# Kernel tuning notes

Hardware: AMD Instinct MI355X
Metric: run time of the kernel (lower is better)

## Reference

```python
import jax, jax.numpy as jnp
import numpy as np

S, B, D, L = 100, 2048, 128, 2  # seq_len, batch, dim_model, n_layers
LN_EPS = 1e-5


def _layer_norm(x, g, b):
    # x: [S, B, D]; normalize over last dim (nn.LayerNorm(dim))
    mu = jnp.mean(x, axis=-1, keepdims=True)
    var = jnp.mean(jnp.square(x - mu), axis=-1, keepdims=True)
    return (x - mu) * jax.lax.rsqrt(var + LN_EPS) * g + b


def _asb(x, cw, cwh, thr):
    # Adaptive_Spectral_Block. x: [S, B, D] -> permute to [B, N, C]
    xb = jnp.transpose(x, (1, 0, 2)).astype(jnp.float32)  # [B, N, C]
    N = xb.shape[1]
    x_fft = jnp.fft.rfft(xb, axis=1, norm='ortho')  # [B, F, C] complex, F = N//2+1
    w = jax.lax.complex(cw[:, 0], cw[:, 1])          # [C]
    x_weighted = x_fft * w
    # adaptive high-frequency mask
    energy = jnp.sum(jnp.square(jnp.abs(x_fft)), axis=-1)  # [B, F]
    F = energy.shape[1]
    # torch.median returns the LOWER of the two middle values -> k-th smallest, k=(F-1)//2
    median = jnp.sort(energy, axis=1)[:, (F - 1) // 2][:, None]  # [B, 1]
    norm_e = energy / (median + 1e-6)
    threshold = jnp.quantile(norm_e, thr)  # global scalar quantile (linear interp, as torch)
    mask = (norm_e < threshold)[..., None].astype(x_fft.real.dtype)  # [B, F, 1]
    wh = jax.lax.complex(cwh[:, 0], cwh[:, 1])       # [C]
    x_weighted = x_weighted + (x_fft * mask) * wh
    out = jnp.fft.irfft(x_weighted, n=N, axis=1, norm='ortho')  # [B, N, C]
    return jnp.transpose(out, (1, 0, 2)).astype(x.dtype)  # back to [S, B, D]


def setup_inputs() -> dict:
    key = jax.random.key(0)
    k0, k1, k2, k3 = jax.random.split(key, 4)
    return {
        'x': jax.random.normal(k0, (S, B, D), dtype=jnp.float32),
        'complex_weight': jax.random.normal(k1, (L, D, 2), dtype=jnp.float32) * 0.02,
        'complex_weight_high': jax.random.normal(k2, (L, D, 2), dtype=jnp.float32) * 0.02,
        'threshold_param': jax.random.uniform(k3, (L,), dtype=jnp.float32) * 0.5,
        'gamma': jnp.ones((L, D), dtype=jnp.float32),
        'beta': jnp.zeros((L, D), dtype=jnp.float32),
    }


def reference(x, complex_weight, complex_weight_high, threshold_param, gamma, beta):
    # Encoder.forward: nlayers x (x = x + ASB(LayerNorm(x)))
    for i in range(L):
        h = _layer_norm(x, gamma[i], beta[i])
        x = x + _asb(h, complex_weight[i], complex_weight_high[i], threshold_param[i])
    return x
```

## Files before the change

kernel.cpp:

```cpp
#include <hip/hip_runtime.h>
#include <math.h>

#define SEQ    100
#define BATCH  2048
#define DIM    128
#define NF     51
#define NLAYER 2
#define MTOT   (BATCH * NF)
#define BD     (BATCH * DIM)
#define XSTR   16384
#define NBQ    96

typedef __attribute__((ext_vector_type(8))) short bf16x8;
typedef __attribute__((ext_vector_type(4))) float f32x4v;

__device__ __forceinline__ unsigned cvtpk(float lo, float hi) {
    unsigned r;
    asm("v_cvt_pk_bf16_f32 %0, %1, %2" : "=v"(r) : "v"(lo), "v"(hi));
    return r;
}
__device__ __forceinline__ unsigned short f2bf(float f) {
    unsigned u = __float_as_uint(f);
    return (unsigned short)((u + 0x7FFFu + ((u >> 16) & 1u)) >> 16);
}
__device__ __forceinline__ float bf2f(unsigned short u) {
    return __uint_as_float((unsigned)u << 16);
}

__global__ void k_tables(unsigned short* __restrict__ imgF,
                         unsigned short* __restrict__ imgI) {
    const int i = blockIdx.x * 256 + threadIdx.x;
    const float W = 6.28318530717958647692f / 100.f;
    if (i < 2 * 64 * 128) {
        const int p = i >> 13, k = (i >> 7) & 63, n = i & 127;
        float v = 0.f;
        if (k < NF && n < SEQ) {
            float s, c; sincosf((float)((k * n) % 100) * W, &s, &c);
            v = 0.1f * (p ? -s : c);
        }
        imgF[i] = f2bf(v);
    }
    if (i < 2 * 128 * 64) {
        const int p = i >> 13, n = (i >> 6) & 127, k = i & 63;
        float v = 0.f;
        if (k < NF && n < SEQ) {
            float s, c; sincosf((float)((k * n) % 100) * W, &s, &c);
            const float a = (k == 0 || k == 50) ? 0.1f : 0.2f;
            v = p ? -a * s : a * c;
        }
        imgI[i] = f2bf(v);
    }
}

__device__ __forceinline__ void fwd_mfma_tail(
    unsigned short* hT, const unsigned short* __restrict__ imgF,
    unsigned short* __restrict__ Xg, float* __restrict__ normE,
    int b, int t, int lane, int wv, int g4, int cc)
{
    bf16x8 Bf[2][4];
    #pragma unroll
    for (int ct = 0; ct < 2; ++ct) {
        const int c = wv * 32 + ct * 16 + cc;
        #pragma unroll
        for (int ks = 0; ks < 4; ++ks)
            Bf[ct][ks] = *(const bf16x8*)&hT[c * 128 + (((ks * 4 + g4) ^ (cc >> 1)) << 3)];
    }
    __syncthreads();

    float* epart    = (float*)hT;
    float* energy_s = (float*)hT + 256;
    float* medp     = (float*)hT + 320;

    #pragma unroll
    for (int mt = 0; mt < 4; ++mt) {
        const int kr = mt * 16 + cc;
        f32x4v aR[2], aI[2];
        aR[0] = aR[1] = aI[0] = aI[1] = (f32x4v){0.f, 0.f, 0.f, 0.f};
        #pragma unroll
        for (int ks = 0; ks < 4; ++ks) {
            const int e0 = kr * 128 + ks * 32 + g4 * 8;
            const bf16x8 A0 = *(const bf16x8*)&imgF[e0];
            const bf16x8 A1 = *(const bf16x8*)&imgF[8192 + e0];
            #pragma unroll
            for (int ct = 0; ct < 2; ++ct) {
                aR[ct] = __builtin_amdgcn_mfma_f32_16x16x32_bf16(A0, Bf[ct][ks], aR[ct], 0, 0, 0);
                aI[ct] = __builtin_amdgcn_mfma_f32_16x16x32_bf16(A1, Bf[ct][ks], aI[ct], 0, 0, 0);
            }
        }
        #pragma unroll
        for (int reg = 0; reg < 4; ++reg) {
            float e = aR[0][reg] * aR[0][reg] + aI[0][reg] * aI[0][reg]
                    + aR[1][reg] * aR[1][reg] + aI[1][reg] * aI[1][reg];
            e += __shfl_xor(e, 1, 64); e += __shfl_xor(e, 2, 64);
            e += __shfl_xor(e, 4, 64); e += __shfl_xor(e, 8, 64);
            if (cc == 0) epart[(mt * 16 + g4 * 4 + reg) * 4 + wv] = e;
        }
        #pragma unroll
        for (int ct = 0; ct < 2; ++ct) {
            const int c = wv * 32 + ct * 16 + cc;
            unsigned short* Xb = Xg + (size_t)b * XSTR + (size_t)c * 128;
            const int k0 = mt * 16 + g4 * 4;
            uint2 pr, pi;
            pr.x = cvtpk(aR[ct][0], aR[ct][1]); pr.y = cvtpk(aR[ct][2], aR[ct][3]);
            pi.x = cvtpk(aI[ct][0], aI[ct][1]); pi.y = cvtpk(aI[ct][2], aI[ct][3]);
            *(uint2*)&Xb[k0]      = pr;
            *(uint2*)&Xb[64 + k0] = pi;
        }
    }
    __syncthreads();
    if (t < 64) energy_s[t] = epart[4 * t] + epart[4 * t + 1]
                            + epart[4 * t + 2] + epart[4 * t + 3];
    __syncthreads();
    if (t < NF) {
        const float e = energy_s[t];
        int cnt = 0;
        for (int j = 0; j < NF; ++j) {
            const float ej = energy_s[j];
            cnt += (ej < e || (ej == e && j < t)) ? 1 : 0;
        }
        if (cnt == (NF - 1) / 2) *medp = e;
    }
    __syncthreads();
    if (t < NF) normE[b * NF + t] = energy_s[t] / (*medp + 1e-6f);
}

__global__ __launch_bounds__(256, 5) void k_fwd(
    const float* __restrict__ x,
    const float* __restrict__ gamma, const float* __restrict__ beta,
    const unsigned short* __restrict__ imgF,
    unsigned short* __restrict__ Xg,
    float* __restrict__ normE)
{
    __shared__ __align__(16) unsigned short hT[128 * 128];

    const int b = blockIdx.x, t = threadIdx.x;
    const int lane = t & 63, wv = t >> 6, g4 = lane >> 4, cc = lane & 15;

    {
        const int c0 = lane * 2;
        const float2 gv = *(const float2*)&gamma[c0];
        const float2 bv = *(const float2*)&beta[c0];
        float2 v[4][8];
        #pragma unroll
        for (int slot = 0; slot < 4; ++slot) {
            const int n0 = (slot * 4 + wv) * 8;
            #pragma unroll
            for (int j = 0; j < 8; ++j)
                if (n0 + j < SEQ)
                    v[slot][j] = *(const float2*)&x[(size_t)(n0 + j) * BD + (size_t)b * DIM + c0];
        }
        #pragma unroll
        for (int slot = 0; slot < 4; ++slot) {
            const int chunk = slot * 4 + wv;
            const int n0 = chunk * 8;
            float he[8], ho[8];
            #pragma unroll
            for (int j = 0; j < 8; ++j) {
                he[j] = 0.f; ho[j] = 0.f;
                if (n0 + j < SEQ) {
                    float s  = v[slot][j].x + v[slot][j].y;
                    float s2 = fmaf(v[slot][j].x, v[slot][j].x, v[slot][j].y * v[slot][j].y);
                    #pragma unroll
                    for (int off = 1; off < 64; off <<= 1) {
                        s  += __shfl_xor(s,  off, 64);
                        s2 += __shfl_xor(s2, off, 64);
                    }
                    const float mu   = s * (1.f / 128.f);
                    const float rstd = rsqrtf(s2 * (1.f / 128.f) - mu * mu + 1e-5f);
                    he[j] = fmaf((v[slot][j].x - mu) * rstd, gv.x, bv.x);
                    ho[j] = fmaf((v[slot][j].y - mu) * rstd, gv.y, bv.y);
                }
            }
            int4 ve, vo;
            ve.x = (int)cvtpk(he[0], he[1]); ve.y = (int)cvtpk(he[2], he[3]);
            ve.z = (int)cvtpk(he[4], he[5]); ve.w = (int)cvtpk(he[6], he[7]);
            vo.x = (int)cvtpk(ho[0], ho[1]); vo.y = (int)cvtpk(ho[2], ho[3]);
            vo.z = (int)cvtpk(ho[4], ho[5]); vo.w = (int)cvtpk(ho[6], ho[7]);
            const int sw = (chunk ^ (lane & 7)) << 3;
            *(int4*)&hT[(c0    ) * 128 + sw] = ve;
            *(int4*)&hT[(c0 + 1) * 128 + sw] = vo;
        }
    }
    __syncthreads();
    fwd_mfma_tail(hT, imgF, Xg, normE, b, t, lane, wv, g4, cc);
}

__device__ __forceinline__ void gbar(unsigned* slot) {
    __syncthreads();
    __threadfence();
    if (threadIdx.x == 0) {
        __hip_atomic_fetch_add(slot, 1u, __ATOMIC_ACQ_REL, __HIP_MEMORY_SCOPE_AGENT);
        while (__hip_atomic_load(slot, __ATOMIC_ACQUIRE, __HIP_MEMORY_SCOPE_AGENT) < NBQ)
            __builtin_amdgcn_s_sleep(8);
    }
    __syncthreads();
}

__device__ __forceinline__ void scan2(const unsigned* __restrict__ H0,
                                      int bins, int shift, bool entry,
                                      unsigned r0, unsigned* sp, unsigned* sc)
{
    const int t = threadIdx.x;
    if (t < 128) {
        const int j = t >> 6, ln = t & 63;
        const unsigned rk = r0 + (unsigned)j;
        const unsigned oldsp = entry ? sp[j] : 0u;
        const unsigned oldsc = entry ? sc[j] : 0u;
        const unsigned rem = rk - oldsc;
        const unsigned* H = H0 + (entry ? j * bins : 0);
        const int per = bins / 64;
        unsigned sum = 0;
        for (int i = 0; i < per; ++i)
            sum += __hip_atomic_load(&H[ln * per + i], __ATOMIC_RELAXED, __HIP_MEMORY_SCOPE_AGENT);
        unsigned pre = sum;
        #pragma unroll
        for (int off = 1; off < 64; off <<= 1) {
            const unsigned tt = __shfl_up(pre, off, 64);
            if (ln >= off) pre += tt;
        }
        const unsigned excl = pre - sum;
        if (rem >= excl && rem < excl + sum) {
            unsigned cum = excl;
            for (int i = 0; i < per; ++i) {
                const unsigned hc = __hip_atomic_load(&H[ln * per + i],
                                        __ATOMIC_RELAXED, __HIP_MEMORY_SCOPE_AGENT);
                if (rem < cum + hc) {
                    sp[j] = oldsp | ((unsigned)(ln * per + i) << shift);
                    sc[j] = oldsc + cum;
                    break;
                }
                cum += hc;
            }
        }
    }
    __syncthreads();
}

__global__ void k_quant(const float* __restrict__ normE,
                        unsigned* __restrict__ hist,
                        unsigned* __restrict__ counters,
                        const float* __restrict__ thrp,
                        const int layer,
                        float* __restrict__ thresh)
{
    __shared__ unsigned lh[4096];
    __shared__ unsigned sp[2], sc[2];
    const int t = threadIdx.x, bid = blockIdx.x;
    const float q = thrp[layer] * (float)(MTOT - 1);
    const unsigned r0 = (unsigned)floorf(q);
    unsigned* cnt = counters + layer * 4;

    for (int i = bid * 256 + t; i < 8192; i += NBQ * 256) hist[i] = 0u;
    gbar(cnt + 0);

    for (int i = t; i < 2048; i += 256) lh[i] = 0;
    __syncthreads();
    for (int i = bid * 256 + t; i < MTOT; i += NBQ * 256)
        atomicAdd(&lh[__float_as_uint(normE[i]) >> 21], 1u);
    __syncthreads();
    for (int i = t; i < 2048; i += 256) {
        const unsigned c = lh[i];
        if (c) atomicAdd(&hist[i], c);
    }
    gbar(cnt + 1);

    scan2(hist, 2048, 21, false, r0, sp, sc);
    {
        const unsigned p0 = sp[0], p1 = sp[1];
        for (int i = t; i < 4096; i += 256) lh[i] = 0;
        __syncthreads();
        for (int i = bid * 256 + t; i < MTOT; i += NBQ * 256) {
            const unsigned v = __float_as_uint(normE[i]);
            const unsigned bin = (v >> 10) & 2047u;
            if ((v & 0xFFE00000u) == p0) atomicAdd(&lh[bin], 1u);
            if ((v & 0xFFE00000u) == p1) atomicAdd(&lh[2048 + bin], 1u);
        }
        __syncthreads();
        for (int i = t; i < 4096; i += 256) {
            const unsigned c = lh[i];
            if (c) atomicAdd(&hist[2048 + i], c);
        }
    }
    gbar(cnt + 2);

    scan2(hist + 2048, 2048, 10, true, r0, sp, sc);
    {
        const unsigned p0 = sp[0], p1 = sp[1];
        for (int i = t; i < 2048; i += 256) lh[i] = 0;
        __syncthreads();
        for (int i = bid * 256 + t; i < MTOT; i += NBQ * 256) {
            const unsigned v = __float_as_uint(normE[i]);
            const unsigned bin = v & 1023u;
            if ((v & 0xFFFFFC00u) == p0) atomicAdd(&lh[bin], 1u);
            if ((v & 0xFFFFFC00u) == p1) atomicAdd(&lh[1024 + bin], 1u);
        }
        __syncthreads();
        for (int i = t; i < 2048; i += 256) {
            const unsigned c = lh[i];
            if (c) atomicAdd(&hist[6144 + i], c);
        }
    }
    gbar(cnt + 3);

    if (bid == 0) {
        scan2(hist + 6144, 1024, 0, true, r0, sp, sc);
        if (t == 0) {
            const float v0 = __uint_as_float(sp[0]);
            const float v1 = __uint_as_float(sp[1]);
            const float frac = q - floorf(q);
            thresh[0] = v0 * (1.f - frac) + v1 * frac;
        }
    }
}

__global__ __launch_bounds__(256, 4) void k_asb_fwd(
    const float* __restrict__ x,
    const float* __restrict__ cw, const float* __restrict__ cwh,
    const unsigned short* __restrict__ imgI,
    const unsigned short* __restrict__ imgF,
    const float* __restrict__ gamma_n, const float* __restrict__ beta_n,
    float* __restrict__ normE,
    const float* __restrict__ thresh,
    float* __restrict__ out,
    unsigned short* __restrict__ Xg)
{
    __shared__ __align__(16) unsigned short hT[128 * 128];
    __shared__ float mask_s[64];
    __shared__ float part_s[112][4], part_q[112][4];
    __shared__ float2 musv[112];

    const int b = blockIdx.x, t = threadIdx.x;
    const int lane = t & 63, wv = t >> 6, g4 = lane >> 4, cc = lane & 15;

    if (t < 64) mask_s[t] = (t < NF && normE[b * NF + t] < thresh[0]) ? 1.f : 0.f;
    __syncthreads();

    bf16x8 Yr[2][2], Yi[2][2];
    float gn[2], bn[2];
    #pragma unroll
    for (int ct = 0; ct < 2; ++ct) {
        const int c = wv * 32 + ct * 16 + cc;
        gn[ct] = gamma_n[c]; bn[ct] = beta_n[c];
        const unsigned short* Xb = Xg + (size_t)b * XSTR + (size_t)c * 128;
        const float2 w2 = *(const float2*)&cw[2 * c];
        const float2 h2 = *(const float2*)&cwh[2 * c];
        #pragma unroll
        for (int kb = 0; kb < 2; ++kb) {
            const bf16x8 xr = *(const bf16x8*)&Xb[kb * 32 + g4 * 8];
            const bf16x8 xi = *(const bf16x8*)&Xb[64 + kb * 32 + g4 * 8];
            float yr[8], yi[8];
            #pragma unroll
            for (int j = 0; j < 8; ++j) {
                const float m   = mask_s[kb * 32 + g4 * 8 + j];
                const float fre = fmaf(m, h2.x, w2.x);
                const float fim = fmaf(m, h2.y, w2.y);
                const float fxr = bf2f((unsigned short)xr[j]);
                const float fxi = bf2f((unsigned short)xi[j]);
                yr[j] = fxr * fre - fxi * fim;
                yi[j] = fxr * fim + fxi * fre;
            }
            unsigned ur[4], ui[4];
            #pragma unroll
            for (int jj = 0; jj < 4; ++jj) {
                ur[jj] = cvtpk(yr[2 * jj], yr[2 * jj + 1]);
                ui[jj] = cvtpk(yi[2 * jj], yi[2 * jj + 1]);
            }
            Yr[ct][kb] = *(bf16x8*)ur;
            Yi[ct][kb] = *(bf16x8*)ui;
        }
    }

    float ov[7][2][4];
    #pragma unroll
    for (int mt = 0; mt < 7; ++mt) {
        const int nr = mt * 16 + cc;
        f32x4v o[2];
        o[0] = o[1] = (f32x4v){0.f, 0.f, 0.f, 0.f};
        #pragma unroll
        for (int kb = 0; kb < 2; ++kb) {
            const int e0 = nr * 64 + kb * 32 + g4 * 8;
            const bf16x8 A0 = *(const bf16x8*)&imgI[e0];
            const bf16x8 A1 = *(const bf16x8*)&imgI[8192 + e0];
            #pragma unroll
            for (int ct = 0; ct < 2; ++ct) {
                o[ct] = __builtin_amdgcn_mfma_f32_16x16x32_bf16(A0, Yr[ct][kb], o[ct], 0, 0, 0);
                o[ct] = __builtin_amdgcn_mfma_f32_16x16x32_bf16(A1, Yi[ct][kb], o[ct], 0, 0, 0);
            }
        }
        #pragma unroll
        for (int ct = 0; ct < 2; ++ct) {
            const int c = wv * 32 + ct * 16 + cc;
            #pragma unroll
            for (int reg = 0; reg < 4; ++reg) {
                const int n = mt * 16 + g4 * 4 + reg;
                float val = 0.f;
                if (n < SEQ) {
                    const size_t idx = (size_t)n * BD + (size_t)b * DIM + c;
                    val = x[idx] + o[ct][reg];
                    out[idx] = val;
                }
                ov[mt][ct][reg] = val;
            }
        }
    }

    #pragma unroll
    for (int mt = 0; mt < 7; ++mt) {
        #pragma unroll
        for (int reg = 0; reg < 4; ++reg) {
            float s  = ov[mt][0][reg] + ov[mt][1][reg];
            float s2 = fmaf(ov[mt][0][reg], ov[mt][0][reg],
                            ov[mt][1][reg] * ov[mt][1][reg]);
            s  += __shfl_xor(s, 1, 64);  s  += __shfl_xor(s, 2, 64);
            s  += __shfl_xor(s, 4, 64);  s  += __shfl_xor(s, 8, 64);
            s2 += __shfl_xor(s2, 1, 64); s2 += __shfl_xor(s2, 2, 64);
            s2 += __shfl_xor(s2, 4, 64); s2 += __shfl_xor(s2, 8, 64);
            if (cc == 0) {
                const int n = mt * 16 + g4 * 4 + reg;
                part_s[n][wv] = s; part_q[n][wv] = s2;
            }
        }
    }
    __syncthreads();
    if (t < 112) {
        const float s  = part_s[t][0] + part_s[t][1] + part_s[t][2] + part_s[t][3];
        const float sq = part_q[t][0] + part_q[t][1] + part_q[t][2] + part_q[t][3];
        const float mu = s * (1.f / 128.f);
        const float rstd = rsqrtf(sq * (1.f / 128.f) - mu * mu + 1e-5f);
        musv[t] = make_float2(mu, rstd);
    }
    __syncthreads();

    {
        const int cf = t >> 1, chf = 14 + (t & 1);
        *(int4*)&hT[cf * 128 + ((chf ^ ((cf >> 1) & 7)) << 3)] = (int4){0, 0, 0, 0};
    }
    #pragma unroll
    for (int mt = 0; mt < 7; ++mt) {
        #pragma unroll
        for (int ct = 0; ct < 2; ++ct) {
            const int c = wv * 32 + ct * 16 + cc;
            #pragma unroll
            for (int pr = 0; pr < 2; ++pr) {
                const int n0 = mt * 16 + g4 * 4 + pr * 2;
                float h0 = 0.f, h1 = 0.f;
                if (n0 < SEQ) {
                    const float2 ms = musv[n0];
                    h0 = fmaf((ov[mt][ct][pr * 2] - ms.x) * ms.y, gn[ct], bn[ct]);
                }
                if (n0 + 1 < SEQ) {
                    const float2 ms = musv[n0 + 1];
                    h1 = fmaf((ov[mt][ct][pr * 2 + 1] - ms.x) * ms.y, gn[ct], bn[ct]);
                }
                const unsigned u = cvtpk(h0, h1);
                const int e = c * 128 + (((n0 >> 3) ^ ((c >> 1) & 7)) << 3) + (n0 & 7);
                *(unsigned*)&hT[e] = u;
            }
        }
    }
    __syncthreads();

    fwd_mfma_tail(hT, imgF, Xg, normE, b, t, lane, wv, g4, cc);
}

__global__ __launch_bounds__(256, 4) void k_asb(
    const float* __restrict__ x,
    const float* __restrict__ cw, const float* __restrict__ cwh,
    const unsigned short* __restrict__ Xg,
    const unsigned short* __restrict__ imgI,
    const float* __restrict__ normE, const float* __restrict__ thresh,
    float* __restrict__ out)
{
    __shared__ __align__(16) float mask_s[64];

    const int b = blockIdx.x, t = threadIdx.x;
    const int lane = t & 63, wv = t >> 6, g4 = lane >> 4, cc = lane & 15;

    if (t < 64) mask_s[t] = (t < NF && normE[b * NF + t] < thresh[0]) ? 1.f : 0.f;
    __syncthreads();

    bf16x8 Yr[2][2], Yi[2][2];
    #pragma unroll
    for (int ct = 0; ct < 2; ++ct) {
        const int c = wv * 32 + ct * 16 + cc;
        const unsigned short* Xb = Xg + (size_t)b * XSTR + (size_t)c * 128;
        const float2 w2 = *(const float2*)&cw[2 * c];
        const float2 h2 = *(const float2*)&cwh[2 * c];
        #pragma unroll
        for (int kb = 0; kb < 2; ++kb) {
            const bf16x8 xr = *(const bf16x8*)&Xb[kb * 32 + g4 * 8];
            const bf16x8 xi = *(const bf16x8*)&Xb[64 + kb * 32 + g4 * 8];
            float yr[8], yi[8];
            #pragma unroll
            for (int j = 0; j < 8; ++j) {
                const float m   = mask_s[kb * 32 + g4 * 8 + j];
                const float fre = fmaf(m, h2.x, w2.x);
                const float fim = fmaf(m, h2.y, w2.y);
                const float fxr = bf2f((unsigned short)xr[j]);
                const float fxi = bf2f((unsigned short)xi[j]);
                yr[j] = fxr * fre - fxi * fim;
                yi[j] = fxr * fim + fxi * fre;
            }
            unsigned ur[4], ui[4];
            #pragma unroll
            for (int jj = 0; jj < 4; ++jj) {
                ur[jj] = cvtpk(yr[2 * jj], yr[2 * jj + 1]);
                ui[jj] = cvtpk(yi[2 * jj], yi[2 * jj + 1]);
            }
            Yr[ct][kb] = *(bf16x8*)ur;
            Yi[ct][kb] = *(bf16x8*)ui;
        }
    }

    #pragma unroll
    for (int mt = 0; mt < 7; ++mt) {
        const int nr = mt * 16 + cc;
        f32x4v o[2];
        o[0] = o[1] = (f32x4v){0.f, 0.f, 0.f, 0.f};
        #pragma unroll
        for (int kb = 0; kb < 2; ++kb) {
            const int e0 = nr * 64 + kb * 32 + g4 * 8;
            const bf16x8 A0 = *(const bf16x8*)&imgI[e0];
            const bf16x8 A1 = *(const bf16x8*)&imgI[8192 + e0];
            #pragma unroll
            for (int ct = 0; ct < 2; ++ct) {
                o[ct] = __builtin_amdgcn_mfma_f32_16x16x32_bf16(A0, Yr[ct][kb], o[ct], 0, 0, 0);
                o[ct] = __builtin_amdgcn_mfma_f32_16x16x32_bf16(A1, Yi[ct][kb], o[ct], 0, 0, 0);
            }
        }
        #pragma unroll
        for (int ct = 0; ct < 2; ++ct) {
            const int c = wv * 32 + ct * 16 + cc;
            #pragma unroll
            for (int reg = 0; reg < 4; ++reg) {
                const int n = mt * 16 + g4 * 4 + reg;
                if (n < SEQ) {
                    const size_t idx = (size_t)n * BD + (size_t)b * DIM + c;
                    out[idx] = x[idx] + o[ct][reg];
                }
            }
        }
    }
}

extern "C" void kernel_launch(void* const* d_in, const int* in_sizes, int n_in,
                              void* d_out, int out_size, void* d_ws, size_t ws_size,
                              hipStream_t stream)
{
    (void)in_sizes; (void)n_in; (void)out_size; (void)ws_size;
    const float* x    = (const float*)d_in[0];
    const float* cw   = (const float*)d_in[1];
    const float* cwh  = (const float*)d_in[2];
    const float* thrp = (const float*)d_in[3];
    const float* gam  = (const float*)d_in[4];
    const float* bet  = (const float*)d_in[5];
    float* out = (float*)d_out;

    char* ws = (char*)d_ws;
    unsigned short* imgF = (unsigned short*)(ws);
    unsigned short* imgI = (unsigned short*)(ws + 32768);
    unsigned short* Xg   = (unsigned short*)(ws + 65536);
    float* normE       = (float*)(ws + 65536 + 67108864);
    unsigned* hist     = (unsigned*)(ws + 65536 + 67108864 + 417792);
    unsigned* counters = (unsigned*)(ws + 65536 + 67108864 + 417792 + 32768);
    float* thresh      = (float*)(ws + 65536 + 67108864 + 417792 + 32768 + 64);

    k_tables<<<64, 256, 0, stream>>>(imgF, imgI);
    (void)hipMemsetAsync(counters, 0, 64, stream);

    k_fwd<<<BATCH, 256, 0, stream>>>(x, gam, bet, imgF, Xg, normE);
    k_quant<<<NBQ, 256, 0, stream>>>(normE, hist, counters, thrp, 0, thresh);
    k_asb_fwd<<<BATCH, 256, 0, stream>>>(x, cw, cwh, imgI, imgF,
                                         gam + DIM, bet + DIM,
                                         normE, thresh, out, Xg);
    k_quant<<<NBQ, 256, 0, stream>>>(normE, hist, counters, thrp, 1, thresh);
    k_asb<<<BATCH, 256, 0, stream>>>(out, cw + DIM * 2, cwh + DIM * 2,
                                     Xg, imgI, normE, thresh, out);
}
```

Before: 425.0 us.

## Replace grid-barrier quantile kernel with separate histogram and last-block select kernels

```diff
diff --git a/kernel.cpp b/kernel.cpp
--- a/kernel.cpp
+++ b/kernel.cpp
@@ -9,7 +9,6 @@
 #define MTOT   (BATCH * NF)
 #define BD     (BATCH * DIM)
 #define XSTR   16384
-#define NBQ    96
 
 typedef __attribute__((ext_vector_type(8))) short bf16x8;
 typedef __attribute__((ext_vector_type(4))) float f32x4v;
@@ -52,79 +51,7 @@
     }
 }
 
-__device__ __forceinline__ void fwd_mfma_tail(
-    unsigned short* hT, const unsigned short* __restrict__ imgF,
-    unsigned short* __restrict__ Xg, float* __restrict__ normE,
-    int b, int t, int lane, int wv, int g4, int cc)
-{
-    bf16x8 Bf[2][4];
-    #pragma unroll
-    for (int ct = 0; ct < 2; ++ct) {
-        const int c = wv * 32 + ct * 16 + cc;
-        #pragma unroll
-        for (int ks = 0; ks < 4; ++ks)
-            Bf[ct][ks] = *(const bf16x8*)&hT[c * 128 + (((ks * 4 + g4) ^ (cc >> 1)) << 3)];
-    }
-    __syncthreads();
-
-    float* epart    = (float*)hT;
-    float* energy_s = (float*)hT + 256;
-    float* medp     = (float*)hT + 320;
-
-    #pragma unroll
-    for (int mt = 0; mt < 4; ++mt) {
-        const int kr = mt * 16 + cc;
-        f32x4v aR[2], aI[2];
-        aR[0] = aR[1] = aI[0] = aI[1] = (f32x4v){0.f, 0.f, 0.f, 0.f};
-        #pragma unroll
-        for (int ks = 0; ks < 4; ++ks) {
-            const int e0 = kr * 128 + ks * 32 + g4 * 8;
-            const bf16x8 A0 = *(const bf16x8*)&imgF[e0];
-            const bf16x8 A1 = *(const bf16x8*)&imgF[8192 + e0];
-            #pragma unroll
-            for (int ct = 0; ct < 2; ++ct) {
-                aR[ct] = __builtin_amdgcn_mfma_f32_16x16x32_bf16(A0, Bf[ct][ks], aR[ct], 0, 0, 0);
-                aI[ct] = __builtin_amdgcn_mfma_f32_16x16x32_bf16(A1, Bf[ct][ks], aI[ct], 0, 0, 0);
-            }
-        }
-        #pragma unroll
-        for (int reg = 0; reg < 4; ++reg) {
-            float e = aR[0][reg] * aR[0][reg] + aI[0][reg] * aI[0][reg]
-                    + aR[1][reg] * aR[1][reg] + aI[1][reg] * aI[1][reg];
-            e += __shfl_xor(e, 1, 64); e += __shfl_xor(e, 2, 64);
-            e += __shfl_xor(e, 4, 64); e += __shfl_xor(e, 8, 64);
-            if (cc == 0) epart[(mt * 16 + g4 * 4 + reg) * 4 + wv] = e;
-        }
-        #pragma unroll
-        for (int ct = 0; ct < 2; ++ct) {
-            const int c = wv * 32 + ct * 16 + cc;
-            unsigned short* Xb = Xg + (size_t)b * XSTR + (size_t)c * 128;
-            const int k0 = mt * 16 + g4 * 4;
-            uint2 pr, pi;
-            pr.x = cvtpk(aR[ct][0], aR[ct][1]); pr.y = cvtpk(aR[ct][2], aR[ct][3]);
-            pi.x = cvtpk(aI[ct][0], aI[ct][1]); pi.y = cvtpk(aI[ct][2], aI[ct][3]);
-            *(uint2*)&Xb[k0]      = pr;
-            *(uint2*)&Xb[64 + k0] = pi;
-        }
-    }
-    __syncthreads();
-    if (t < 64) energy_s[t] = epart[4 * t] + epart[4 * t + 1]
-                            + epart[4 * t + 2] + epart[4 * t + 3];
-    __syncthreads();
-    if (t < NF) {
-        const float e = energy_s[t];
-        int cnt = 0;
-        for (int j = 0; j < NF; ++j) {
-            const float ej = energy_s[j];
-            cnt += (ej < e || (ej == e && j < t)) ? 1 : 0;
-        }
-        if (cnt == (NF - 1) / 2) *medp = e;
-    }
-    __syncthreads();
-    if (t < NF) normE[b * NF + t] = energy_s[t] / (*medp + 1e-6f);
-}
-
-__global__ __launch_bounds__(256, 5) void k_fwd(
+__global__ __launch_bounds__(256, 4) void k_fwd(
     const float* __restrict__ x,
     const float* __restrict__ gamma, const float* __restrict__ beta,
     const unsigned short* __restrict__ imgF,
@@ -132,6 +59,9 @@
     float* __restrict__ normE)
 {
     __shared__ __align__(16) unsigned short hT[128 * 128];
+    __shared__ float epart[64][4];
+    __shared__ float energy_s[64];
+    __shared__ float med_s;
 
     const int b = blockIdx.x, t = threadIdx.x;
     const int lane = t & 63, wv = t >> 6, g4 = lane >> 4, cc = lane & 15;
@@ -182,32 +112,155 @@
         }
     }
     __syncthreads();
-    fwd_mfma_tail(hT, imgF, Xg, normE, b, t, lane, wv, g4, cc);
-}
-
-__device__ __forceinline__ void gbar(unsigned* slot) {
-    __syncthreads();
+
+    bf16x8 Bf[2][4];
+    #pragma unroll
+    for (int ct = 0; ct < 2; ++ct) {
+        const int c = wv * 32 + ct * 16 + cc;
+        #pragma unroll
+        for (int ks = 0; ks < 4; ++ks)
+            Bf[ct][ks] = *(const bf16x8*)&hT[c * 128 + (((ks * 4 + g4) ^ (cc >> 1)) << 3)];
+    }
+
+    #pragma unroll
+    for (int mt = 0; mt < 4; ++mt) {
+        const int kr = mt * 16 + cc;
+        f32x4v aR[2], aI[2];
+        aR[0] = aR[1] = aI[0] = aI[1] = (f32x4v){0.f, 0.f, 0.f, 0.f};
+        #pragma unroll
+        for (int ks = 0; ks < 4; ++ks) {
+            const int e0 = kr * 128 + ks * 32 + g4 * 8;
+            const bf16x8 A0 = *(const bf16x8*)&imgF[e0];
+            const bf16x8 A1 = *(const bf16x8*)&imgF[8192 + e0];
+            #pragma unroll
+            for (int ct = 0; ct < 2; ++ct) {
+                aR[ct] = __builtin_amdgcn_mfma_f32_16x16x32_bf16(A0, Bf[ct][ks], aR[ct], 0, 0, 0);
+                aI[ct] = __builtin_amdgcn_mfma_f32_16x16x32_bf16(A1, Bf[ct][ks], aI[ct], 0, 0, 0);
+            }
+        }
+        #pragma unroll
+        for (int reg = 0; reg < 4; ++reg) {
+            float e = aR[0][reg] * aR[0][reg] + aI[0][reg] * aI[0][reg]
+                    + aR[1][reg] * aR[1][reg] + aI[1][reg] * aI[1][reg];
+            e += __shfl_xor(e, 1, 64); e += __shfl_xor(e, 2, 64);
+            e += __shfl_xor(e, 4, 64); e += __shfl_xor(e, 8, 64);
+            if (cc == 0) epart[mt * 16 + g4 * 4 + reg][wv] = e;
+        }
+        #pragma unroll
+        for (int ct = 0; ct < 2; ++ct) {
+            const int c = wv * 32 + ct * 16 + cc;
+            unsigned short* Xb = Xg + (size_t)b * XSTR + (size_t)c * 128;
+            const int k0 = mt * 16 + g4 * 4;
+            uint2 pr, pi;
+            pr.x = cvtpk(aR[ct][0], aR[ct][1]); pr.y = cvtpk(aR[ct][2], aR[ct][3]);
+            pi.x = cvtpk(aI[ct][0], aI[ct][1]); pi.y = cvtpk(aI[ct][2], aI[ct][3]);
+            *(uint2*)&Xb[k0]      = pr;
+            *(uint2*)&Xb[64 + k0] = pi;
+        }
+    }
+    __syncthreads();
+    if (t < 64) energy_s[t] = epart[t][0] + epart[t][1] + epart[t][2] + epart[t][3];
+    __syncthreads();
+    if (t < NF) {
+        const float e = energy_s[t];
+        int cnt = 0;
+        for (int j = 0; j < NF; ++j) {
+            const float ej = energy_s[j];
+            cnt += (ej < e || (ej == e && j < t)) ? 1 : 0;
+        }
+        if (cnt == (NF - 1) / 2) med_s = e;
+    }
+    __syncthreads();
+    if (t < NF) normE[b * NF + t] = energy_s[t] / (med_s + 1e-6f);
+}
+
+__global__ void k_hist0(const float* __restrict__ normE,
+                        unsigned* __restrict__ hist)
+{
+    __shared__ unsigned lh[2048];
+    for (int i = threadIdx.x; i < 2048; i += 256) lh[i] = 0;
+    __syncthreads();
+    for (int i = blockIdx.x * 256 + threadIdx.x; i < MTOT; i += gridDim.x * 256)
+        atomicAdd(&lh[__float_as_uint(normE[i]) >> 21], 1u);
+    __syncthreads();
+    for (int i = threadIdx.x; i < 2048; i += 256) {
+        const unsigned c = lh[i];
+        if (c) atomicAdd(&hist[i], c);
+    }
+}
+
+__global__ void k_sel(const float* __restrict__ normE,
+                      unsigned* __restrict__ hist,
+                      unsigned* __restrict__ sel,
+                      unsigned* __restrict__ done,
+                      const float* __restrict__ thrp,
+                      const int layer, const int phase,
+                      float* __restrict__ thresh)
+{
+    __shared__ unsigned lh[4096];
+    __shared__ unsigned sp[2], sc[2];
+    __shared__ unsigned ticket_s;
+    __shared__ float vb[2];
+    const int t = threadIdx.x;
+    const float q = thrp[layer] * (float)(MTOT - 1);
+    const unsigned r0 = (unsigned)floorf(q);
+
+    if (phase == 1) {
+        if (t < 128) {
+            const int j = t >> 6, ln = t & 63;
+            const unsigned rk = r0 + (unsigned)j;
+            unsigned sum = 0;
+            for (int i = 0; i < 32; ++i) sum += hist[ln * 32 + i];
+            unsigned pre = sum;
+            #pragma unroll
+            for (int off = 1; off < 64; off <<= 1) {
+                const unsigned tt = __shfl_up(pre, off, 64);
+                if (ln >= off) pre += tt;
+            }
+            const unsigned excl = pre - sum;
+            if (rk >= excl && rk < excl + sum) {
+                unsigned cum = excl;
+                for (int i = 0; i < 32; ++i) {
+                    const unsigned hc = hist[ln * 32 + i];
+                    if (rk < cum + hc) { sp[j] = (unsigned)(ln * 32 + i) << 21; sc[j] = cum; break; }
+                    cum += hc;
+                }
+            }
+        }
+    } else {
+        if (t < 2) { sp[t] = sel[2 * t]; sc[t] = sel[2 * t + 1]; }
+    }
+    __syncthreads();
+    const unsigned p0 = sp[0], p1 = sp[1];
+    const int bins      = (phase == 1) ? 2048 : 1024;
+    const int shift     = (phase == 1) ? 10 : 0;
+    const unsigned hmsk = (phase == 1) ? 0xFFE00000u : 0xFFFFFC00u;
+    const int region    = (phase == 1) ? 2048 : 6144;
+
+    for (int i = t; i < 2 * bins; i += 256) lh[i] = 0;
+    __syncthreads();
+    for (int i = blockIdx.x * 256 + t; i < MTOT; i += gridDim.x * 256) {
+        const unsigned v = __float_as_uint(normE[i]);
+        const unsigned bin = (v >> shift) & (unsigned)(bins - 1);
+        if ((v & hmsk) == p0) atomicAdd(&lh[bin], 1u);
+        if ((v & hmsk) == p1) atomicAdd(&lh[bins + bin], 1u);
+    }
+    __syncthreads();
+    for (int i = t; i < 2 * bins; i += 256) {
+        const unsigned c = lh[i];
+        if (c) atomicAdd(&hist[region + i], c);
+    }
     __threadfence();
-    if (threadIdx.x == 0) {
-        __hip_atomic_fetch_add(slot, 1u, __ATOMIC_ACQ_REL, __HIP_MEMORY_SCOPE_AGENT);
-        while (__hip_atomic_load(slot, __ATOMIC_ACQUIRE, __HIP_MEMORY_SCOPE_AGENT) < NBQ)
-            __builtin_amdgcn_s_sleep(8);
-    }
-    __syncthreads();
-}
-
-__device__ __forceinline__ void scan2(const unsigned* __restrict__ H0,
-                                      int bins, int shift, bool entry,
-                                      unsigned r0, unsigned* sp, unsigned* sc)
-{
-    const int t = threadIdx.x;
+    if (t == 0) ticket_s = atomicAdd(&done[(layer << 1) + (phase - 1)], 1u);
+    __syncthreads();
+    if (ticket_s != (unsigned)(gridDim.x - 1)) return;
+    __threadfence();
+
     if (t < 128) {
         const int j = t >> 6, ln = t & 63;
-        const unsigned rk = r0 + (unsigned)j;
-        const unsigned oldsp = entry ? sp[j] : 0u;
-        const unsigned oldsc = entry ? sc[j] : 0u;
-        const unsigned rem = rk - oldsc;
-        const unsigned* H = H0 + (entry ? j * bins : 0);
+        const unsigned rk  = r0 + (unsigned)j;
+        const unsigned rem = rk - sc[j];
+        const unsigned* H  = hist + region + j * bins;
         const int per = bins / 64;
         unsigned sum = 0;
         for (int i = 0; i < per; ++i)
@@ -225,8 +278,9 @@
                 const unsigned hc = __hip_atomic_load(&H[ln * per + i],
                                         __ATOMIC_RELAXED, __HIP_MEMORY_SCOPE_AGENT);
                 if (rem < cum + hc) {
-                    sp[j] = oldsp | ((unsigned)(ln * per + i) << shift);
-                    sc[j] = oldsc + cum;
+                    const unsigned bin = (unsigned)(ln * per + i);
+                    if (phase == 1) { sel[2 * j] = sp[j] | (bin << 10); sel[2 * j + 1] = sc[j] + cum; }
+                    else            vb[j] = __uint_as_float(sp[j] | bin);
                     break;
                 }
                 cum += hc;
@@ -234,82 +288,11 @@
         }
     }
     __syncthreads();
-}
-
-__global__ void k_quant(const float* __restrict__ normE,
-                        unsigned* __restrict__ hist,
-                        unsigned* __restrict__ counters,
-                        const float* __restrict__ thrp,
-                        const int layer,
-                        float* __restrict__ thresh)
-{
-    __shared__ unsigned lh[4096];
-    __shared__ unsigned sp[2], sc[2];
-    const int t = threadIdx.x, bid = blockIdx.x;
-    const float q = thrp[layer] * (float)(MTOT - 1);
-    const unsigned r0 = (unsigned)floorf(q);
-    unsigned* cnt = counters + layer * 4;
-
-    for (int i = bid * 256 + t; i < 8192; i += NBQ * 256) hist[i] = 0u;
-    gbar(cnt + 0);
-
-    for (int i = t; i < 2048; i += 256) lh[i] = 0;
-    __syncthreads();
-    for (int i = bid * 256 + t; i < MTOT; i += NBQ * 256)
-        atomicAdd(&lh[__float_as_uint(normE[i]) >> 21], 1u);
-    __syncthreads();
-    for (int i = t; i < 2048; i += 256) {
-        const unsigned c = lh[i];
-        if (c) atomicAdd(&hist[i], c);
-    }
-    gbar(cnt + 1);
-
-    scan2(hist, 2048, 21, false, r0, sp, sc);
-    {
-        const unsigned p0 = sp[0], p1 = sp[1];
-        for (int i = t; i < 4096; i += 256) lh[i] = 0;
-        __syncthreads();
-        for (int i = bid * 256 + t; i < MTOT; i += NBQ * 256) {
-            const unsigned v = __float_as_uint(normE[i]);
-            const unsigned bin = (v >> 10) & 2047u;
-            if ((v & 0xFFE00000u) == p0) atomicAdd(&lh[bin], 1u);
-            if ((v & 0xFFE00000u) == p1) atomicAdd(&lh[2048 + bin], 1u);
-        }
-        __syncthreads();
-        for (int i = t; i < 4096; i += 256) {
-            const unsigned c = lh[i];
-            if (c) atomicAdd(&hist[2048 + i], c);
-        }
-    }
-    gbar(cnt + 2);
-
-    scan2(hist + 2048, 2048, 10, true, r0, sp, sc);
-    {
-        const unsigned p0 = sp[0], p1 = sp[1];
-        for (int i = t; i < 2048; i += 256) lh[i] = 0;
-        __syncthreads();
-        for (int i = bid * 256 + t; i < MTOT; i += NBQ * 256) {
-            const unsigned v = __float_as_uint(normE[i]);
-            const unsigned bin = v & 1023u;
-            if ((v & 0xFFFFFC00u) == p0) atomicAdd(&lh[bin], 1u);
-            if ((v & 0xFFFFFC00u) == p1) atomicAdd(&lh[1024 + bin], 1u);
-        }
-        __syncthreads();
-        for (int i = t; i < 2048; i += 256) {
-            const unsigned c = lh[i];
-            if (c) atomicAdd(&hist[6144 + i], c);
-        }
-    }
-    gbar(cnt + 3);
-
-    if (bid == 0) {
-        scan2(hist + 6144, 1024, 0, true, r0, sp, sc);
-        if (t == 0) {
-            const float v0 = __uint_as_float(sp[0]);
-            const float v1 = __uint_as_float(sp[1]);
-            const float frac = q - floorf(q);
-            thresh[0] = v0 * (1.f - frac) + v1 * frac;
-        }
+    if (phase == 1) { for (int i = t; i < 6144; i += 256) hist[i] = 0u; }
+    else            { for (int i = t; i < 2048; i += 256) hist[6144 + i] = 0u; }
+    if (t == 0 && phase == 2) {
+        const float frac = q - floorf(q);
+        thresh[0] = vb[0] * (1.f - frac) + vb[1] * frac;
     }
 }
 
@@ -460,7 +443,73 @@
     }
     __syncthreads();
 
-    fwd_mfma_tail(hT, imgF, Xg, normE, b, t, lane, wv, g4, cc);
+    {
+        bf16x8 Bf[2][4];
+        #pragma unroll
+        for (int ct = 0; ct < 2; ++ct) {
+            const int c = wv * 32 + ct * 16 + cc;
+            #pragma unroll
+            for (int ks = 0; ks < 4; ++ks)
+                Bf[ct][ks] = *(const bf16x8*)&hT[c * 128 + (((ks * 4 + g4) ^ (cc >> 1)) << 3)];
+        }
+        __syncthreads();
+
+        float* epart    = (float*)hT;
+        float* energy_s = (float*)hT + 256;
+        float* medp     = (float*)hT + 320;
+
+        #pragma unroll
+        for (int mt = 0; mt < 4; ++mt) {
+            const int kr = mt * 16 + cc;
+            f32x4v aR[2], aI[2];
+            aR[0] = aR[1] = aI[0] = aI[1] = (f32x4v){0.f, 0.f, 0.f, 0.f};
+            #pragma unroll
+            for (int ks = 0; ks < 4; ++ks) {
+                const int e0 = kr * 128 + ks * 32 + g4 * 8;
+                const bf16x8 A0 = *(const bf16x8*)&imgF[e0];
+                const bf16x8 A1 = *(const bf16x8*)&imgF[8192 + e0];
+                #pragma unroll
+                for (int ct = 0; ct < 2; ++ct) {
+                    aR[ct] = __builtin_amdgcn_mfma_f32_16x16x32_bf16(A0, Bf[ct][ks], aR[ct], 0, 0, 0);
+                    aI[ct] = __builtin_amdgcn_mfma_f32_16x16x32_bf16(A1, Bf[ct][ks], aI[ct], 0, 0, 0);
+                }
+            }
+            #pragma unroll
+            for (int reg = 0; reg < 4; ++reg) {
+                float e = aR[0][reg] * aR[0][reg] + aI[0][reg] * aI[0][reg]
+                        + aR[1][reg] * aR[1][reg] + aI[1][reg] * aI[1][reg];
+                e += __shfl_xor(e, 1, 64); e += __shfl_xor(e, 2, 64);
+                e += __shfl_xor(e, 4, 64); e += __shfl_xor(e, 8, 64);
+                if (cc == 0) epart[(mt * 16 + g4 * 4 + reg) * 4 + wv] = e;
+            }
+            #pragma unroll
+            for (int ct = 0; ct < 2; ++ct) {
+                const int c = wv * 32 + ct * 16 + cc;
+                unsigned short* Xb = Xg + (size_t)b * XSTR + (size_t)c * 128;
+                const int k0 = mt * 16 + g4 * 4;
+                uint2 pr, pi;
+                pr.x = cvtpk(aR[ct][0], aR[ct][1]); pr.y = cvtpk(aR[ct][2], aR[ct][3]);
+                pi.x = cvtpk(aI[ct][0], aI[ct][1]); pi.y = cvtpk(aI[ct][2], aI[ct][3]);
+                *(uint2*)&Xb[k0]      = pr;
+                *(uint2*)&Xb[64 + k0] = pi;
+            }
+        }
+        __syncthreads();
+        if (t < 64) energy_s[t] = epart[4 * t] + epart[4 * t + 1]
+                                + epart[4 * t + 2] + epart[4 * t + 3];
+        __syncthreads();
+        if (t < NF) {
+            const float e = energy_s[t];
+            int cnt = 0;
+            for (int j = 0; j < NF; ++j) {
+                const float ej = energy_s[j];
+                cnt += (ej < e || (ej == e && j < t)) ? 1 : 0;
+            }
+            if (cnt == (NF - 1) / 2) *medp = e;
+        }
+        __syncthreads();
+        if (t < NF) normE[b * NF + t] = energy_s[t] / (*medp + 1e-6f);
+    }
 }
 
 __global__ __launch_bounds__(256, 4) void k_asb(
@@ -560,20 +609,25 @@
     unsigned short* imgF = (unsigned short*)(ws);
     unsigned short* imgI = (unsigned short*)(ws + 32768);
     unsigned short* Xg   = (unsigned short*)(ws + 65536);
-    float* normE       = (float*)(ws + 65536 + 67108864);
-    unsigned* hist     = (unsigned*)(ws + 65536 + 67108864 + 417792);
-    unsigned* counters = (unsigned*)(ws + 65536 + 67108864 + 417792 + 32768);
-    float* thresh      = (float*)(ws + 65536 + 67108864 + 417792 + 32768 + 64);
+    float* normE    = (float*)(ws + 65536 + 67108864);
+    unsigned* hist  = (unsigned*)(ws + 65536 + 67108864 + 417792);
+    unsigned* done  = (unsigned*)(ws + 65536 + 67108864 + 417792 + 32768);
+    unsigned* sel   = (unsigned*)(ws + 65536 + 67108864 + 417792 + 32768 + 64);
+    float* thresh   = (float*)(ws + 65536 + 67108864 + 417792 + 32768 + 128);
 
     k_tables<<<64, 256, 0, stream>>>(imgF, imgI);
-    (void)hipMemsetAsync(counters, 0, 64, stream);
+    (void)hipMemsetAsync(hist, 0, 32768 + 64, stream);
 
     k_fwd<<<BATCH, 256, 0, stream>>>(x, gam, bet, imgF, Xg, normE);
-    k_quant<<<NBQ, 256, 0, stream>>>(normE, hist, counters, thrp, 0, thresh);
+    k_hist0<<<96, 256, 0, stream>>>(normE, hist);
+    k_sel<<<96, 256, 0, stream>>>(normE, hist, sel, done, thrp, 0, 1, thresh);
+    k_sel<<<96, 256, 0, stream>>>(normE, hist, sel, done, thrp, 0, 2, thresh);
     k_asb_fwd<<<BATCH, 256, 0, stream>>>(x, cw, cwh, imgI, imgF,
                                          gam + DIM, bet + DIM,
                                          normE, thresh, out, Xg);
-    k_quant<<<NBQ, 256, 0, stream>>>(normE, hist, counters, thrp, 1, thresh);
+    k_hist0<<<96, 256, 0, stream>>>(normE, hist);
+    k_sel<<<96, 256, 0, stream>>>(normE, hist, sel, done, thrp, 1, 1, thresh);
+    k_sel<<<96, 256, 0, stream>>>(normE, hist, sel, done, thrp, 1, 2, thresh);
     k_asb<<<BATCH, 256, 0, stream>>>(out, cw + DIM * 2, cwh + DIM * 2,
                                      Xg, imgI, normE, thresh, out);
 }
```

New measurement: 399.8 us. -5.9%, faster.
